# Kernel optimization log

Measured on AMD Instinct MI355X. Metric: run time of the kernel, lower is better.

The kernel has to match this reference:

```python
import jax, jax.numpy as jnp
import numpy as np

NH = 16   # neighbors
MD = 64   # model_dim
FF = 128  # ff_dim
H = 4     # heads
HD = MD // H
B, S, T = 2, 8192, 4096
LOG100 = float(np.log(100.0))


def _ln(x, g, b, eps=1e-5):
    m = x.mean(-1, keepdims=True)
    v = ((x - m) ** 2).mean(-1, keepdims=True)
    return (x - m) * jax.lax.rsqrt(v + eps) * g + b


def _lrelu(x):
    return jnp.where(x >= 0, x, 0.2 * x)


def setup_inputs():
    ks = jax.random.split(jax.random.key(0), 16)
    rn = lambda k, sh: jax.random.normal(k, sh, dtype=jnp.float32) * 0.05
    return {
        "x": jax.random.normal(ks[0], (B, S, 1), dtype=jnp.float32),
        "c1": jax.random.normal(ks[1], (B, S, T), dtype=jnp.float32),
        "c2": jax.random.normal(ks[2], (B, S, T), dtype=jnp.float32),
        "pe_W1": rn(ks[3], (2, FF)), "pe_b1": jnp.zeros((FF,), jnp.float32),
        "pe_W2": rn(ks[4], (FF, MD)), "pe_b2": jnp.zeros((MD,), jnp.float32),
        "Wq": rn(ks[5], (MD, MD)), "Wk": rn(ks[6], (MD, MD)), "Wv": rn(ks[7], (1, MD)),
        "logit_scale": jnp.full((H, 1, 1), float(np.log(10.0)), jnp.float32),
        "Wo": rn(ks[8], (MD, MD)), "bo": jnp.zeros((MD,), jnp.float32),
        "g1": jnp.ones((MD,), jnp.float32), "beta1": jnp.zeros((MD,), jnp.float32),
        "g2": jnp.ones((MD,), jnp.float32), "beta2": jnp.zeros((MD,), jnp.float32),
        "g3": jnp.ones((MD * NH,), jnp.float32), "beta3": jnp.zeros((MD * NH,), jnp.float32),
        "mnh_W1": rn(ks[9], (MD, FF)), "mnh_b1": jnp.zeros((FF,), jnp.float32),
        "mnh_W2": rn(ks[10], (FF, 1)), "mnh_b2": jnp.zeros((1,), jnp.float32),
        "mu_W1": rn(ks[11], (MD * NH, MD * NH)), "mu_b1": jnp.zeros((MD * NH,), jnp.float32),
        "mu_W2": rn(ks[12], (MD * NH, MD * NH)), "mu_b2": jnp.zeros((MD * NH,), jnp.float32),
    }


def reference(x, c1, c2, pe_W1, pe_b1, pe_W2, pe_b2, Wq, Wk, Wv, logit_scale, Wo, bo,
              g1, beta1, g2, beta2, g3, beta3,
              mnh_W1, mnh_b1, mnh_W2, mnh_b2, mu_W1, mu_b1, mu_W2, mu_b2):
    b, s, t = c1.shape
    # KNN over source axis s (cartesian distance), per target t
    d = c1 * c1 + c2 * c2                                  # [b,s,t]
    _, idx = jax.lax.top_k(-jnp.swapaxes(d, 1, 2), NH)     # [b,t,NH]
    x_nh = jax.vmap(lambda xb, ib: xb[ib])(x, idx)         # [b,t,NH,e]
    c1g = jnp.take_along_axis(jnp.swapaxes(c1, 1, 2), idx, axis=2)  # [b,t,NH]
    c2g = jnp.take_along_axis(jnp.swapaxes(c2, 1, 2), idx, axis=2)
    # relative-position embedding MLP (PE), already in [b,t,NH,MD] layout
    pe = jnp.stack([c1g, c2g], -1)                         # [b,t,NH,2]
    pe = jax.nn.gelu(pe @ pe_W1 + pe_b1) @ pe_W2 + pe_b2   # [b,t,NH,MD]
    h = _ln(x_nh + pe, g1, beta1).reshape(b * t, NH, MD)   # e=1 broadcasts
    v = jnp.einsum('bne,ed->bnd', x_nh.reshape(b * t, NH, 1), Wv)
    q = h @ Wq
    k = h @ Wk
    sp = lambda z: z.reshape(b * t, NH, H, HD).transpose(0, 2, 1, 3)
    qh, kh, vh = sp(q), sp(k), sp(v)
    # logit-scaled (cosine) attention over the NH neighbor axis
    qn = qh * jax.lax.rsqrt(jnp.sum(qh * qh, -1, keepdims=True) + 1e-12)
    kn = kh * jax.lax.rsqrt(jnp.sum(kh * kh, -1, keepdims=True) + 1e-12)
    scale = jnp.exp(jnp.minimum(logit_scale, LOG100))      # [H,1,1]
    att = jax.nn.softmax(jnp.einsum('bhnd,bhmd->bhnm', qn, kn) * scale, axis=-1)
    o = jnp.einsum('bhnm,bhmd->bhnd', att, vh).transpose(0, 2, 1, 3).reshape(b * t, NH, MD)
    h = _ln(h + (o @ Wo + bo), g2, beta2)
    # per-neighbor MLP producing a scalar, broadcast-added back
    h = h + _lrelu(_lrelu(h @ mnh_W1 + mnh_b1) @ mnh_W2 + mnh_b2)
    # unfold neighbors into channels and run the unfold MLP
    h = _ln(h.reshape(b, t, NH * MD), g3, beta3)
    return _lrelu(_lrelu(h @ mu_W1 + mu_b1) @ mu_W2 + mu_b2)  # [b,t,NH*MD]
```

## Files before the change

kernel.cpp:

```cpp
#include <hip/hip_runtime.h>
#include <hip/hip_bf16.h>

#define B_    2
#define SSRC  8192
#define TT    4096
#define NHN   16
#define NC    64
#define CS    128
#define LOG100D 4.605170185988091368035982909368

typedef short s16x8 __attribute__((ext_vector_type(8)));
typedef float f32x4 __attribute__((ext_vector_type(4)));
typedef double f64x4 __attribute__((ext_vector_type(4)));
typedef unsigned long long u64;

typedef const __attribute__((address_space(1))) void* gas_ptr;
typedef __attribute__((address_space(3))) void* las_ptr;
#define GLDS16(g, l) __builtin_amdgcn_global_load_lds((gas_ptr)(g), (las_ptr)(l), 16, 0, 0)

#define WFENCE asm volatile("s_waitcnt lgkmcnt(0)" ::: "memory")

__device__ __forceinline__ unsigned short f2bf(float f) {
    unsigned u = __float_as_uint(f);
    u = u + 0x7fffu + ((u >> 16) & 1u);
    return (unsigned short)(u >> 16);
}
__device__ __forceinline__ float bf2f(unsigned short h) {
    return __uint_as_float(((unsigned)h) << 16);
}
__device__ __forceinline__ double lrelu_d(double v) { return v >= 0.0 ? v : 0.2 * v; }
__device__ __forceinline__ double gelu_d(double u) {
    double a = 0.7978845608028654 * (u + 0.044715 * u * u * u);
    return 0.5 * u * (1.0 + tanh(a));
}
__device__ __forceinline__ double rsum16d(double v) {
    v += __shfl_xor(v, 1); v += __shfl_xor(v, 2);
    v += __shfl_xor(v, 4); v += __shfl_xor(v, 8);
    return v;
}
__device__ __forceinline__ double rmax16d(double v) {
    v = fmax(v, __shfl_xor(v, 1)); v = fmax(v, __shfl_xor(v, 2));
    v = fmax(v, __shfl_xor(v, 4)); v = fmax(v, __shfl_xor(v, 8));
    return v;
}
__device__ __forceinline__ double rsum64d(double v) {
    v += __shfl_xor(v, 1); v += __shfl_xor(v, 2); v += __shfl_xor(v, 4);
    v += __shfl_xor(v, 8); v += __shfl_xor(v, 16); v += __shfl_xor(v, 32);
    return v;
}

__device__ __forceinline__ int mfma64_discover() {
    int lane = threadIdx.x & 63;
    int l15 = lane & 15, lg = lane >> 4;
    double va = (double)(1 + ((lane * 37) % 61));
    double vb = (double)(2 + ((lane * 53) % 59));
    f64x4 d = (f64x4){0.0, 0.0, 0.0, 0.0};
    d = __builtin_amdgcn_mfma_f64_16x16x4f64(va, vb, d, 0, 0, 0);
    int found = -1;
#pragma unroll
    for (int c = 0; c < 8; c++) {
        int dm = (c >> 2) & 1, am = (c >> 1) & 1, bm = c & 1;
        bool ok = true;
#pragma unroll
        for (int r = 0; r < 4; r++) {
            int i = dm ? (lg + 4 * r) : (4 * lg + r);
            int j = l15;
            double e = 0.0;
#pragma unroll
            for (int k = 0; k < 4; k++) {
                int la = am ? (4 * i + k) : (i + 16 * k);
                int lb = bm ? (4 * j + k) : (j + 16 * k);
                e += (double)(1 + ((la * 37) % 61)) * (double)(2 + ((lb * 53) % 59));
            }
            ok = ok && (d[r] == e);
        }
        if (__all(ok) && found < 0) found = c;
    }
    return found;
}

__device__ __forceinline__ void ce(u64 &a, u64 &b) {
    bool c = a < b; u64 lo = c ? a : b; u64 hi = c ? b : a; a = lo; b = hi;
}
__device__ __forceinline__ void sort16(u64 (&k)[16]) {
    ce(k[0],k[8]); ce(k[1],k[9]); ce(k[2],k[10]); ce(k[3],k[11]);
    ce(k[4],k[12]); ce(k[5],k[13]); ce(k[6],k[14]); ce(k[7],k[15]);
    ce(k[0],k[4]); ce(k[1],k[5]); ce(k[2],k[6]); ce(k[3],k[7]);
    ce(k[8],k[12]); ce(k[9],k[13]); ce(k[10],k[14]); ce(k[11],k[15]);
    ce(k[4],k[8]); ce(k[5],k[9]); ce(k[6],k[10]); ce(k[7],k[11]);
    ce(k[0],k[2]); ce(k[1],k[3]); ce(k[4],k[6]); ce(k[5],k[7]);
    ce(k[8],k[10]); ce(k[9],k[11]); ce(k[12],k[14]); ce(k[13],k[15]);
    ce(k[2],k[8]); ce(k[3],k[9]); ce(k[6],k[12]); ce(k[7],k[13]);
    ce(k[2],k[4]); ce(k[3],k[5]); ce(k[6],k[8]); ce(k[7],k[9]);
    ce(k[10],k[12]); ce(k[11],k[13]);
    ce(k[0],k[1]); ce(k[2],k[3]); ce(k[4],k[5]); ce(k[6],k[7]);
    ce(k[8],k[9]); ce(k[10],k[11]); ce(k[12],k[13]); ce(k[14],k[15]);
    ce(k[1],k[8]); ce(k[3],k[10]); ce(k[5],k[12]); ce(k[7],k[14]);
    ce(k[1],k[4]); ce(k[3],k[6]); ce(k[5],k[8]); ce(k[7],k[10]);
    ce(k[9],k[12]); ce(k[11],k[14]);
    ce(k[1],k[2]); ce(k[3],k[4]); ce(k[5],k[6]); ce(k[7],k[8]);
    ce(k[9],k[10]); ce(k[11],k[12]); ce(k[13],k[14]);
}
__device__ __forceinline__ void bmerge16(u64 (&k)[16]) {
    ce(k[0],k[8]); ce(k[1],k[9]); ce(k[2],k[10]); ce(k[3],k[11]);
    ce(k[4],k[12]); ce(k[5],k[13]); ce(k[6],k[14]); ce(k[7],k[15]);
    ce(k[0],k[4]); ce(k[1],k[5]); ce(k[2],k[6]); ce(k[3],k[7]);
    ce(k[8],k[12]); ce(k[9],k[13]); ce(k[10],k[14]); ce(k[11],k[15]);
    ce(k[0],k[2]); ce(k[1],k[3]); ce(k[4],k[6]); ce(k[5],k[7]);
    ce(k[8],k[10]); ce(k[9],k[11]); ce(k[12],k[14]); ce(k[13],k[15]);
    ce(k[0],k[1]); ce(k[2],k[3]); ce(k[4],k[5]); ce(k[6],k[7]);
    ce(k[8],k[9]); ce(k[10],k[11]); ce(k[12],k[13]); ce(k[14],k[15]);
}
__device__ __forceinline__ void merge_keep16(u64 (&L)[16], const u64 (&B)[16]) {
#pragma unroll
    for (int i = 0; i < 16; i++) { u64 bb = B[15 - i]; L[i] = L[i] < bb ? L[i] : bb; }
    bmerge16(L);
}

__global__ __launch_bounds__(256) void topk_partial(
    const float* __restrict__ c1, const float* __restrict__ c2,
    u64* __restrict__ cand)
{
    int t = blockIdx.x * 256 + threadIdx.x;
    int ch = blockIdx.y, b = blockIdx.z;
    const float* p1 = c1 + ((size_t)b * SSRC + (size_t)ch * CS) * TT + t;
    const float* p2 = c2 + ((size_t)b * SSRC + (size_t)ch * CS) * TT + t;
    u64 k[16];
#pragma unroll
    for (int j = 0; j < 16; j++) k[j] = ~0ull;
    int sbase = ch * CS;
    for (int s = 0; s < CS; s += 16) {
        u64 bt[16];
#pragma unroll
        for (int u = 0; u < 16; u++) {
            float a_ = p1[(size_t)(s + u) * TT];
            float b_ = p2[(size_t)(s + u) * TT];
            float dd = __fadd_rn(__fmul_rn(a_, a_), __fmul_rn(b_, b_));
            bt[u] = ((u64)__float_as_uint(dd) << 32) | (unsigned)(sbase + s + u);
        }
        sort16(bt);
        merge_keep16(k, bt);
    }
    u64* dst = cand + ((size_t)(b * NC + ch) * 16) * TT + t;
#pragma unroll
    for (int j = 0; j < 16; j++) dst[(size_t)j * TT] = k[j];
}

__global__ __launch_bounds__(64) void topk_merge1(
    const u64* __restrict__ cand, u64* __restrict__ c2c)
{
    int t = blockIdx.x * 64 + threadIdx.x;
    int g = blockIdx.y, b = blockIdx.z;
    u64 k[16];
#pragma unroll
    for (int j = 0; j < 16; j++) k[j] = ~0ull;
    for (int c = g * 8; c < g * 8 + 8; c++) {
        const u64* src = cand + ((size_t)(b * NC + c) * 16) * TT + t;
        u64 bt[16];
#pragma unroll
        for (int j = 0; j < 16; j++) bt[j] = src[(size_t)j * TT];
        merge_keep16(k, bt);
    }
    u64* dst = c2c + ((size_t)((b * 8 + g) * 16)) * TT + t;
#pragma unroll
    for (int j = 0; j < 16; j++) dst[(size_t)j * TT] = k[j];
}

__global__ __launch_bounds__(64) void topk_merge2(
    const u64* __restrict__ c2c, int* __restrict__ knn)
{
    int t = blockIdx.x * 64 + threadIdx.x;
    int b = blockIdx.y;
    u64 k[16];
#pragma unroll
    for (int j = 0; j < 16; j++) k[j] = ~0ull;
    for (int c = 0; c < 8; c++) {
        const u64* src = c2c + ((size_t)(b * 8 + c) * 16) * TT + t;
        u64 bt[16];
#pragma unroll
        for (int j = 0; j < 16; j++) bt[j] = src[(size_t)j * TT];
        merge_keep16(k, bt);
    }
#pragma unroll
    for (int j = 0; j < 16; j++)
        knn[((size_t)b * TT + t) * 16 + j] = (int)(unsigned)(k[j] & 0xffffffffull);
}

__global__ __launch_bounds__(256) void wconv(
    const float* __restrict__ Wa, const float* __restrict__ Wb,
    unsigned short* __restrict__ Oah, unsigned short* __restrict__ Oal,
    unsigned short* __restrict__ Obh, unsigned short* __restrict__ Obl)
{
    const float* W = blockIdx.z ? Wb : Wa;
    unsigned short* Oh = blockIdx.z ? Obh : Oah;
    unsigned short* Ol = blockIdx.z ? Obl : Oal;
    __shared__ float tile[64][65];
    int tx = threadIdx.x & 63, ty = threadIdx.x >> 6;
    int n0 = blockIdx.x * 64, k0 = blockIdx.y * 64;
#pragma unroll
    for (int r = ty; r < 64; r += 4) tile[r][tx] = W[(size_t)(k0 + r) * 1024 + n0 + tx];
    __syncthreads();
#pragma unroll
    for (int r = ty; r < 64; r += 4) {
        float v = tile[tx][r];
        unsigned short hi = f2bf(v);
        Oh[(size_t)(n0 + r) * 1024 + k0 + tx] = hi;
        Ol[(size_t)(n0 + r) * 1024 + k0 + tx] = f2bf(v - bf2f(hi));
    }
}

__global__ __launch_bounds__(256) void tok_pe_m(
    const float* __restrict__ x, const float* __restrict__ c1, const float* __restrict__ c2,
    const int* __restrict__ knn,
    const float* __restrict__ peW1, const float* __restrict__ peb1,
    const float* __restrict__ peW2, const float* __restrict__ peb2,
    const float* __restrict__ g1, const float* __restrict__ be1,
    float* __restrict__ hout)
{
    int cand = mfma64_discover();
    if (cand < 0) return;
    __shared__ float s_peW1[256], s_peb1[128], s_peW2[8448], s_peb2[64], s_g1[64], s_be1[64];
    __shared__ float s_scr[4][2352];
    int tid = threadIdx.x, lane = tid & 63, w = tid >> 6;
    if (tid < 256) s_peW1[tid] = peW1[tid];
    if (tid < 128) s_peb1[tid] = peb1[tid];
    if (tid < 64) { s_peb2[tid] = peb2[tid]; s_g1[tid] = g1[tid]; s_be1[tid] = be1[tid]; }
    for (int i = tid; i < 8192; i += 256) s_peW2[(i >> 6) * 66 + (i & 63)] = peW2[i];
    __syncthreads();

    int l15 = lane & 15, lg = lane >> 4;
    int am = (cand >> 1) & 1, bm = cand & 1, dm = (cand >> 2) & 1;
    int a_i = am ? (lane >> 2) : l15;
    int a_k = am ? (lane & 3)  : lg;
    int b_k = bm ? (lane & 3)  : lg;
    int b_j = bm ? (lane >> 2) : l15;
    int i0 = dm ? lg : 4 * lg;
    int istep = dm ? 4 : 1;

    float* big = s_scr[w];
    float* sc1 = big + 2304; float* sc2 = big + 2320; float* sx = big + 2336;
    double w0a = s_peW1[lane], w1a = s_peW1[128 + lane], ba = s_peb1[lane];
    double w0b = s_peW1[64 + lane], w1b = s_peW1[192 + lane], bbv = s_peb1[64 + lane];
    double g1v[4], be1v[4], pb2v[4];
#pragma unroll
    for (int j = 0; j < 4; j++) {
        g1v[j]  = (double)s_g1[j * 16 + l15];
        be1v[j] = (double)s_be1[j * 16 + l15];
        pb2v[j] = (double)s_peb2[j * 16 + l15];
    }

    for (int it = 0; it < 4; ++it) {
        int tk = blockIdx.x * 16 + w * 4 + it;
        int bb = tk >> 12, tt = tk & (TT - 1);
        if (lane < 16) {
            int s = knn[(size_t)tk * 16 + lane];
            sc1[lane] = c1[((size_t)bb * SSRC + s) * TT + tt];
            sc2[lane] = c2[((size_t)bb * SSRC + s) * TT + tt];
            sx[lane]  = x[bb * SSRC + s];
        }
        WFENCE;
#pragma unroll
        for (int n = 0; n < 16; n++) {
            double a_ = (double)sc1[n], b_ = (double)sc2[n];
            big[lane * 18 + n]        = (float)gelu_d(a_ * w0a + b_ * w1a + ba);
            big[(lane + 64) * 18 + n] = (float)gelu_d(a_ * w0b + b_ * w1b + bbv);
        }
        WFENCE;
        f64x4 acc[4];
#pragma unroll
        for (int j = 0; j < 4; j++) acc[j] = (f64x4){0.0, 0.0, 0.0, 0.0};
        for (int ks = 0; ks < 32; ks++) {
            double a = (double)big[(4 * ks + a_k) * 18 + a_i];
            const float* wrow = &s_peW2[(4 * ks + b_k) * 66 + b_j];
#pragma unroll
            for (int j = 0; j < 4; j++)
                acc[j] = __builtin_amdgcn_mfma_f64_16x16x4f64(a, (double)wrow[j * 16], acc[j], 0, 0, 0);
        }
        float* op = hout + (size_t)tk * 1024;
#pragma unroll
        for (int r = 0; r < 4; r++) {
            int n = i0 + istep * r;
            double xr = (double)sx[n];
            double v[4], s = 0.0;
#pragma unroll
            for (int j = 0; j < 4; j++) { v[j] = acc[j][r] + pb2v[j] + xr; s += v[j]; }
            double m = rsum16d(s) * (1.0 / 64.0);
            double q = 0.0;
#pragma unroll
            for (int j = 0; j < 4; j++) { double d = v[j] - m; q += d * d; }
            double var = rsum16d(q) * (1.0 / 64.0);
            double rs = sqrt(var + 1e-5);
#pragma unroll
            for (int j = 0; j < 4; j++)
                op[n * 64 + j * 16 + l15] = (float)((v[j] - m) / rs * g1v[j] + be1v[j]);
        }
    }
}

__global__ __launch_bounds__(256) void tok_pe_v(
    const float* __restrict__ x, const float* __restrict__ c1, const float* __restrict__ c2,
    const int* __restrict__ knn,
    const float* __restrict__ peW1, const float* __restrict__ peb1,
    const float* __restrict__ peW2, const float* __restrict__ peb2,
    const float* __restrict__ g1, const float* __restrict__ be1,
    float* __restrict__ hout)
{
    int cand = mfma64_discover();
    if (cand >= 0) return;
    __shared__ float s_peW1[256], s_peb1[128], s_peW2[8448], s_peb2[64], s_g1[64], s_be1[64];
    __shared__ float s_scr[4][2352];
    int tid = threadIdx.x, lane = tid & 63, w = tid >> 6;
    if (tid < 256) s_peW1[tid] = peW1[tid];
    if (tid < 128) s_peb1[tid] = peb1[tid];
    if (tid < 64) { s_peb2[tid] = peb2[tid]; s_g1[tid] = g1[tid]; s_be1[tid] = be1[tid]; }
    for (int i = tid; i < 8192; i += 256) s_peW2[(i >> 6) * 66 + (i & 63)] = peW2[i];
    __syncthreads();

    float* big = s_scr[w];
    float* sc1 = big + 2304; float* sc2 = big + 2320; float* sx = big + 2336;
    double w0a = s_peW1[lane], w1a = s_peW1[128 + lane], ba = s_peb1[lane];
    double w0b = s_peW1[64 + lane], w1b = s_peW1[192 + lane], bbv = s_peb1[64 + lane];
    double gv = (double)s_g1[lane], bv = (double)s_be1[lane];
    double pb2 = (double)s_peb2[lane];

    for (int it = 0; it < 4; ++it) {
        int tk = blockIdx.x * 16 + w * 4 + it;
        int bb = tk >> 12, tt = tk & (TT - 1);
        if (lane < 16) {
            int s = knn[(size_t)tk * 16 + lane];
            sc1[lane] = c1[((size_t)bb * SSRC + s) * TT + tt];
            sc2[lane] = c2[((size_t)bb * SSRC + s) * TT + tt];
            sx[lane]  = x[bb * SSRC + s];
        }
        WFENCE;
#pragma unroll
        for (int n = 0; n < 16; n++) {
            double a_ = (double)sc1[n], b_ = (double)sc2[n];
            big[lane * 18 + n]        = (float)gelu_d(a_ * w0a + b_ * w1a + ba);
            big[(lane + 64) * 18 + n] = (float)gelu_d(a_ * w0b + b_ * w1b + bbv);
        }
        WFENCE;
        double acc[16];
#pragma unroll
        for (int n = 0; n < 16; n++) acc[n] = pb2;
        for (int f = 0; f < 128; f++) {
            double wv = (double)s_peW2[f * 66 + lane];
#pragma unroll
            for (int n = 0; n < 16; n += 2) {
                float2 gvv = *(const float2*)&big[f * 18 + n];
                acc[n]     += (double)gvv.x * wv;
                acc[n + 1] += (double)gvv.y * wv;
            }
        }
        float* op = hout + (size_t)tk * 1024 + lane;
#pragma unroll
        for (int n = 0; n < 16; n++) {
            double v = acc[n] + (double)sx[n];
            double m = rsum64d(v) * (1.0 / 64.0);
            double d = v - m;
            double var = rsum64d(d * d) * (1.0 / 64.0);
            op[n * 64] = (float)(d / sqrt(var + 1e-5) * gv + bv);
        }
    }
}

__global__ __launch_bounds__(256) void tok_attn(
    const float* __restrict__ x, const int* __restrict__ knn,
    const float* __restrict__ Wq, const float* __restrict__ Wk,
    const float* __restrict__ Wv, const float* __restrict__ lsc,
    const float* __restrict__ Wo, const float* __restrict__ bo,
    const float* __restrict__ g2, const float* __restrict__ be2,
    float* __restrict__ hio)
{
    __shared__ float s_Wq[4224], s_Wk[4224], s_WoV[256], s_bo[64], s_g2[64], s_be2[64];
    __shared__ float s_scr[4][2320];
    int tid = threadIdx.x, lane = tid & 63, w = tid >> 6;
    if (tid < 64) {
        s_bo[tid] = bo[tid]; s_g2[tid] = g2[tid]; s_be2[tid] = be2[tid];
        for (int hh = 0; hh < 4; hh++) {
            double a = 0.0;
            for (int hd = 0; hd < 16; hd++)
                a += (double)Wv[hh * 16 + hd] * (double)Wo[(hh * 16 + hd) * 64 + tid];
            s_WoV[hh * 64 + tid] = (float)a;
        }
    }
    for (int i = tid; i < 4096; i += 256) {
        s_Wq[(i >> 6) * 66 + (i & 63)] = Wq[i];
        s_Wk[(i >> 6) * 66 + (i & 63)] = Wk[i];
    }
    __syncthreads();

    int head = lane >> 4, mm = lane & 15;
    double scaleh = exp(fmin((double)lsc[head], LOG100D));
    double wov0 = (double)s_WoV[lane], wov1 = (double)s_WoV[64 + lane];
    double wov2 = (double)s_WoV[128 + lane], wov3 = (double)s_WoV[192 + lane];
    double gv = (double)s_g2[lane], bv = (double)s_be2[lane], bov = (double)s_bo[lane];
    float* big = s_scr[w];
    float* sx = big + 2304;

    for (int it = 0; it < 4; ++it) {
        int tk = blockIdx.x * 16 + w * 4 + it;
        int bb = tk >> 12;
        if (lane < 16) {
            int s = knn[(size_t)tk * 16 + lane];
            sx[lane] = x[bb * SSRC + s];
        }
        float* hp = hio + (size_t)tk * 1024 + lane;
        double h[16];
#pragma unroll
        for (int n = 0; n < 16; n++) {
            h[n] = (double)hp[n * 64];
            big[lane * 18 + n] = (float)h[n];
        }
        WFENCE;
        double q[16], k2[16];
#pragma unroll
        for (int n = 0; n < 16; n++) { q[n] = 0.0; k2[n] = 0.0; }
        for (int kk = 0; kk < 64; kk++) {
            double wq = (double)s_Wq[kk * 66 + lane], wk = (double)s_Wk[kk * 66 + lane];
#pragma unroll
            for (int n = 0; n < 16; n += 2) {
                float2 hv = *(const float2*)&big[kk * 18 + n];
                q[n]  += (double)hv.x * wq; q[n + 1]  += (double)hv.y * wq;
                k2[n] += (double)hv.x * wk; k2[n + 1] += (double)hv.y * wk;
            }
        }
#pragma unroll
        for (int n = 0; n < 16; n++) {
            double sq = rsum16d(q[n] * q[n]);   q[n]  /= sqrt(sq + 1e-12);
            double sk = rsum16d(k2[n] * k2[n]); k2[n] /= sqrt(sk + 1e-12);
        }
        WFENCE;
#pragma unroll
        for (int n = 0; n < 16; n++) {
            big[lane * 18 + n]        = (float)q[n];
            big[1152 + lane * 18 + n] = (float)k2[n];
        }
        WFENCE;
        double A_[16];
        {
            double S[16];
#pragma unroll
            for (int n = 0; n < 16; n++) S[n] = 0.0;
            for (int hd = 0; hd < 16; hd++) {
                int r = head * 16 + hd;
                double kf = (double)big[1152 + r * 18 + mm];
#pragma unroll
                for (int n = 0; n < 16; n += 2) {
                    float2 qq = *(const float2*)&big[r * 18 + n];
                    S[n] += (double)qq.x * kf; S[n + 1] += (double)qq.y * kf;
                }
            }
            double xv = (double)sx[mm];
#pragma unroll
            for (int n = 0; n < 16; n++) {
                double sv = S[n] * scaleh;
                double mx = rmax16d(sv);
                double e = exp(sv - mx);
                double se = rsum16d(e);
                A_[n] = rsum16d((e / se) * xv);
            }
        }
#pragma unroll
        for (int n = 0; n < 16; n++) {
            double a0 = __shfl(A_[n], mm), a1 = __shfl(A_[n], 16 + mm);
            double a2 = __shfl(A_[n], 32 + mm), a3 = __shfl(A_[n], 48 + mm);
            double v = h[n] + a0 * wov0 + a1 * wov1 + a2 * wov2 + a3 * wov3 + bov;
            double m = rsum64d(v) * (1.0 / 64.0);
            double d = v - m;
            double var = rsum64d(d * d) * (1.0 / 64.0);
            hp[n * 64] = (float)(d / sqrt(var + 1e-5) * gv + bv);
        }
    }
}

__global__ __launch_bounds__(256) void tok_mnh_m(
    const float* __restrict__ hin,
    const float* __restrict__ mW1, const float* __restrict__ mb1,
    const float* __restrict__ mW2, const float* __restrict__ mb2,
    const float* __restrict__ g3, const float* __restrict__ be3,
    unsigned short* __restrict__ hnh, unsigned short* __restrict__ hnl)
{
    int cand = mfma64_discover();
    if (cand < 0) return;
    __shared__ float s_mW1[8320], s_mb1[128], s_mW2[128], s_g3[1024], s_be3[1024];
    __shared__ float s_scr[4][1152];
    int tid = threadIdx.x, lane = tid & 63, w = tid >> 6;
    if (tid < 128) { s_mb1[tid] = mb1[tid]; s_mW2[tid] = mW2[tid]; }
    for (int i = tid; i < 8192; i += 256) s_mW1[(i >> 7) * 130 + (i & 127)] = mW1[i];
    for (int i = tid; i < 1024; i += 256) { s_g3[i] = g3[i]; s_be3[i] = be3[i]; }
    __syncthreads();

    int l15 = lane & 15, lg = lane >> 4;
    int am = (cand >> 1) & 1, bm = cand & 1, dm = (cand >> 2) & 1;
    int a_i = am ? (lane >> 2) : l15;
    int a_k = am ? (lane & 3)  : lg;
    int b_k = bm ? (lane & 3)  : lg;
    int b_j = bm ? (lane >> 2) : l15;

    double mb2s = (double)mb2[0];
    double mb1v[8], w2v[8];
#pragma unroll
    for (int j = 0; j < 8; j++) {
        mb1v[j] = (double)s_mb1[j * 16 + l15];
        w2v[j]  = (double)s_mW2[j * 16 + l15];
    }
    float* big = s_scr[w];

    for (int it = 0; it < 4; ++it) {
        int tk = blockIdx.x * 16 + w * 4 + it;
        const float* hp = hin + (size_t)tk * 1024 + lane;
        double h[16];
#pragma unroll
        for (int n = 0; n < 16; n++) {
            h[n] = (double)hp[n * 64];
            big[lane * 18 + n] = (float)h[n];
        }
        WFENCE;
        f64x4 acc[8];
#pragma unroll
        for (int j = 0; j < 8; j++) acc[j] = (f64x4){0.0, 0.0, 0.0, 0.0};
        for (int ks = 0; ks < 16; ks++) {
            double a = (double)big[(4 * ks + a_k) * 18 + a_i];
            const float* wrow = &s_mW1[(4 * ks + b_k) * 130 + b_j];
#pragma unroll
            for (int j = 0; j < 8; j++)
                acc[j] = __builtin_amdgcn_mfma_f64_16x16x4f64(a, (double)wrow[j * 16], acc[j], 0, 0, 0);
        }
        double p[4];
#pragma unroll
        for (int r = 0; r < 4; r++) {
            double s = 0.0;
#pragma unroll
            for (int j = 0; j < 8; j++) {
                double t = acc[j][r] + mb1v[j];
                s += lrelu_d(t) * w2v[j];
            }
            p[r] = rsum16d(s);
        }
        if (dm == 0) {
#pragma unroll
            for (int n = 0; n < 16; n++) {
                double pn = __shfl(p[n & 3], (n >> 2) * 16);
                h[n] += lrelu_d(pn + mb2s);
            }
        } else {
#pragma unroll
            for (int n = 0; n < 16; n++) {
                double pn = __shfl(p[n >> 2], (n & 3) * 16);
                h[n] += lrelu_d(pn + mb2s);
            }
        }
        double s1 = 0.0;
#pragma unroll
        for (int n = 0; n < 16; n++) s1 += h[n];
        s1 = rsum64d(s1) * (1.0 / 1024.0);
        double s2v = 0.0;
#pragma unroll
        for (int n = 0; n < 16; n++) { double d = h[n] - s1; s2v += d * d; }
        s2v = rsum64d(s2v) * (1.0 / 1024.0);
        double rs = 1.0 / sqrt(s2v + 1e-5);
        unsigned short* oph = hnh + (size_t)tk * 1024 + lane;
        unsigned short* opl = hnl + (size_t)tk * 1024 + lane;
#pragma unroll
        for (int n = 0; n < 16; n++) {
            double v = (h[n] - s1) * rs * (double)s_g3[n * 64 + lane] + (double)s_be3[n * 64 + lane];
            unsigned short hi = f2bf((float)v);
            oph[n * 64] = hi;
            opl[n * 64] = f2bf((float)(v - (double)bf2f(hi)));
        }
    }
}

__global__ __launch_bounds__(256) void tok_mnh_v(
    const float* __restrict__ hin,
    const float* __restrict__ mW1, const float* __restrict__ mb1,
    const float* __restrict__ mW2, const float* __restrict__ mb2,
    const float* __restrict__ g3, const float* __restrict__ be3,
    unsigned short* __restrict__ hnh, unsigned short* __restrict__ hnl)
{
    int cand = mfma64_discover();
    if (cand >= 0) return;
    __shared__ float s_mW1[8320], s_mb1[128], s_mW2[128], s_g3[1024], s_be3[1024];
    __shared__ float s_scr[4][1152];
    int tid = threadIdx.x, lane = tid & 63, w = tid >> 6;
    if (tid < 128) { s_mb1[tid] = mb1[tid]; s_mW2[tid] = mW2[tid]; }
    for (int i = tid; i < 8192; i += 256) s_mW1[(i >> 7) * 130 + (i & 127)] = mW1[i];
    for (int i = tid; i < 1024; i += 256) { s_g3[i] = g3[i]; s_be3[i] = be3[i]; }
    __syncthreads();

    double mb2s = (double)mb2[0];
    double mb1a = (double)s_mb1[lane], mb1b = (double)s_mb1[64 + lane];
    double w2a = (double)s_mW2[lane], w2b = (double)s_mW2[64 + lane];
    float* big = s_scr[w];

    for (int it = 0; it < 4; ++it) {
        int tk = blockIdx.x * 16 + w * 4 + it;
        const float* hp = hin + (size_t)tk * 1024 + lane;
        double h[16];
#pragma unroll
        for (int n = 0; n < 16; n++) {
            h[n] = (double)hp[n * 64];
            big[lane * 18 + n] = (float)h[n];
        }
        WFENCE;
        double t1a[16], t1b[16];
#pragma unroll
        for (int n = 0; n < 16; n++) { t1a[n] = mb1a; t1b[n] = mb1b; }
        for (int kk = 0; kk < 64; kk++) {
            double wa = (double)s_mW1[kk * 130 + lane], wb = (double)s_mW1[kk * 130 + 64 + lane];
#pragma unroll
            for (int n = 0; n < 16; n += 2) {
                float2 hv = *(const float2*)&big[kk * 18 + n];
                t1a[n] += (double)hv.x * wa; t1a[n + 1] += (double)hv.y * wa;
                t1b[n] += (double)hv.x * wb; t1b[n + 1] += (double)hv.y * wb;
            }
        }
#pragma unroll
        for (int n = 0; n < 16; n++) {
            double p = lrelu_d(t1a[n]) * w2a + lrelu_d(t1b[n]) * w2b;
            p = rsum64d(p);
            h[n] += lrelu_d(p + mb2s);
        }
        double s1 = 0.0;
#pragma unroll
        for (int n = 0; n < 16; n++) s1 += h[n];
        s1 = rsum64d(s1) * (1.0 / 1024.0);
        double s2v = 0.0;
#pragma unroll
        for (int n = 0; n < 16; n++) { double d = h[n] - s1; s2v += d * d; }
        s2v = rsum64d(s2v) * (1.0 / 1024.0);
        double rs = 1.0 / sqrt(s2v + 1e-5);
        unsigned short* oph = hnh + (size_t)tk * 1024 + lane;
        unsigned short* opl = hnl + (size_t)tk * 1024 + lane;
#pragma unroll
        for (int n = 0; n < 16; n++) {
            double v = (h[n] - s1) * rs * (double)s_g3[n * 64 + lane] + (double)s_be3[n * 64 + lane];
            unsigned short hi = f2bf((float)v);
            oph[n * 64] = hi;
            opl[n * 64] = f2bf((float)(v - (double)bf2f(hi)));
        }
    }
}

#define AH_OFF 0
#define AL_OFF 4096
#define BH_OFF 8192
#define BL_OFF 12288
template<int OUTSPLIT>
__global__ __launch_bounds__(256) void gemm_split(
    const unsigned short* __restrict__ Ah, const unsigned short* __restrict__ Al,
    const unsigned short* __restrict__ Bh, const unsigned short* __restrict__ Bl,
    const float* __restrict__ bias,
    unsigned short* __restrict__ oh, unsigned short* __restrict__ ol,
    float* __restrict__ of, int M, int N, int K)
{
    __shared__ unsigned short SM[16384];
    int tid = threadIdx.x, lane = tid & 63, w = tid >> 6;
    int wm = w >> 1, wn = w & 1;
    int m0 = blockIdx.y * 128, n0 = blockIdx.x * 128;
    f32x4 acc[4][4];
#pragma unroll
    for (int i = 0; i < 4; i++)
#pragma unroll
        for (int j = 0; j < 4; j++) acc[i][j] = (f32x4){0.f, 0.f, 0.f, 0.f};
    int row = tid >> 2, c8 = (tid & 3) * 8;
    size_t aoff = (size_t)(m0 + row) * K + c8;
    size_t boff = (size_t)(n0 + row) * K + c8;
    for (int kk = 0; kk < K; kk += 32) {
        __syncthreads();
        GLDS16(Ah + aoff + kk,                   SM + AH_OFF + tid * 8);
        GLDS16(Ah + aoff + (size_t)64 * K + kk,  SM + AH_OFF + 2048 + tid * 8);
        GLDS16(Al + aoff + kk,                   SM + AL_OFF + tid * 8);
        GLDS16(Al + aoff + (size_t)64 * K + kk,  SM + AL_OFF + 2048 + tid * 8);
        GLDS16(Bh + boff + kk,                   SM + BH_OFF + tid * 8);
        GLDS16(Bh + boff + (size_t)64 * K + kk,  SM + BH_OFF + 2048 + tid * 8);
        GLDS16(Bl + boff + kk,                   SM + BL_OFF + tid * 8);
        GLDS16(Bl + boff + (size_t)64 * K + kk,  SM + BL_OFF + 2048 + tid * 8);
        asm volatile("s_waitcnt vmcnt(0)" ::: "memory");
        __syncthreads();
        int kh = (lane >> 4) * 8, rA = wm * 64 + (lane & 15), rB = wn * 64 + (lane & 15);
        s16x8 afh[4], afl[4], bfh[4], bfl[4];
#pragma unroll
        for (int i = 0; i < 4; i++) {
            afh[i] = *(const s16x8*)&SM[AH_OFF + (rA + i * 16) * 32 + kh];
            afl[i] = *(const s16x8*)&SM[AL_OFF + (rA + i * 16) * 32 + kh];
            bfh[i] = *(const s16x8*)&SM[BH_OFF + (rB + i * 16) * 32 + kh];
            bfl[i] = *(const s16x8*)&SM[BL_OFF + (rB + i * 16) * 32 + kh];
        }
#pragma unroll
        for (int i = 0; i < 4; i++)
#pragma unroll
            for (int j = 0; j < 4; j++) {
                acc[i][j] = __builtin_amdgcn_mfma_f32_16x16x32_bf16(afl[i], bfh[j], acc[i][j], 0, 0, 0);
                acc[i][j] = __builtin_amdgcn_mfma_f32_16x16x32_bf16(afh[i], bfl[j], acc[i][j], 0, 0, 0);
                acc[i][j] = __builtin_amdgcn_mfma_f32_16x16x32_bf16(afh[i], bfh[j], acc[i][j], 0, 0, 0);
            }
    }
    float bc[4];
#pragma unroll
    for (int j = 0; j < 4; j++) bc[j] = bias[n0 + wn * 64 + j * 16 + (lane & 15)];
#pragma unroll
    for (int i = 0; i < 4; i++) {
#pragma unroll
        for (int j = 0; j < 4; j++) {
#pragma unroll
            for (int r = 0; r < 4; r++) {
                int rw = m0 + wm * 64 + i * 16 + (lane >> 4) * 4 + r;
                int cl = n0 + wn * 64 + j * 16 + (lane & 15);
                float v = acc[i][j][r] + bc[j];
                v = v >= 0.f ? v : 0.2f * v;
                if (OUTSPLIT) {
                    unsigned short hi = f2bf(v);
                    oh[(size_t)rw * N + cl] = hi;
                    ol[(size_t)rw * N + cl] = f2bf(v - bf2f(hi));
                } else {
                    of[(size_t)rw * N + cl] = v;
                }
            }
        }
    }
}

extern "C" void kernel_launch(void* const* d_in, const int* in_sizes, int n_in,
                              void* d_out, int out_size, void* d_ws, size_t ws_size,
                              hipStream_t stream)
{
    const float* x    = (const float*)d_in[0];
    const float* c1   = (const float*)d_in[1];
    const float* c2   = (const float*)d_in[2];
    const float* peW1 = (const float*)d_in[3];
    const float* peb1 = (const float*)d_in[4];
    const float* peW2 = (const float*)d_in[5];
    const float* peb2 = (const float*)d_in[6];
    const float* Wq   = (const float*)d_in[7];
    const float* Wk   = (const float*)d_in[8];
    const float* Wv   = (const float*)d_in[9];
    const float* lsc  = (const float*)d_in[10];
    const float* Wo   = (const float*)d_in[11];
    const float* bo   = (const float*)d_in[12];
    const float* g1   = (const float*)d_in[13];
    const float* be1  = (const float*)d_in[14];
    const float* g2   = (const float*)d_in[15];
    const float* be2  = (const float*)d_in[16];
    const float* g3   = (const float*)d_in[17];
    const float* be3  = (const float*)d_in[18];
    const float* mW1  = (const float*)d_in[19];
    const float* mb1  = (const float*)d_in[20];
    const float* mW2  = (const float*)d_in[21];
    const float* mb2  = (const float*)d_in[22];
    const float* muW1 = (const float*)d_in[23];
    const float* mub1 = (const float*)d_in[24];
    const float* muW2 = (const float*)d_in[25];
    const float* mub2 = (const float*)d_in[26];

    const size_t MB = (size_t)1 << 20;
    char* ws = (char*)d_ws;
    u64*            cand   = (u64*)(ws);
    float*          hbuf   = (float*)(ws);
    unsigned short* y1h    = (unsigned short*)(ws);
    unsigned short* y1l    = (unsigned short*)(ws + 16 * MB);
    unsigned short* hnh    = (unsigned short*)(ws + 32 * MB);
    unsigned short* hnl    = (unsigned short*)(ws + 48 * MB);
    u64*            c2c    = (u64*)(ws + 64 * MB);
    unsigned short* w1th   = (unsigned short*)(ws + 72 * MB);
    unsigned short* w1tl   = (unsigned short*)(ws + 74 * MB);
    unsigned short* w2th   = (unsigned short*)(ws + 76 * MB);
    unsigned short* w2tl   = (unsigned short*)(ws + 78 * MB);
    int*            knn    = (int*)(ws + 80 * MB);
    (void)in_sizes; (void)n_in; (void)out_size; (void)ws_size;

    wconv<<<dim3(16, 16, 2), 256, 0, stream>>>(muW1, muW2, w1th, w1tl, w2th, w2tl);
    topk_partial<<<dim3(TT / 256, NC, B_), 256, 0, stream>>>(c1, c2, cand);
    topk_merge1<<<dim3(TT / 64, 8, B_), 64, 0, stream>>>(cand, c2c);
    topk_merge2<<<dim3(TT / 64, B_), 64, 0, stream>>>(c2c, knn);
    tok_pe_m<<<dim3(512), 256, 0, stream>>>(x, c1, c2, knn, peW1, peb1, peW2, peb2, g1, be1, hbuf);
    tok_pe_v<<<dim3(512), 256, 0, stream>>>(x, c1, c2, knn, peW1, peb1, peW2, peb2, g1, be1, hbuf);
    tok_attn<<<dim3(512), 256, 0, stream>>>(x, knn, Wq, Wk, Wv, lsc, Wo, bo, g2, be2, hbuf);
    tok_mnh_m<<<dim3(512), 256, 0, stream>>>(hbuf, mW1, mb1, mW2, mb2, g3, be3, hnh, hnl);
    tok_mnh_v<<<dim3(512), 256, 0, stream>>>(hbuf, mW1, mb1, mW2, mb2, g3, be3, hnh, hnl);
    gemm_split<1><<<dim3(8, 64), 256, 0, stream>>>(hnh, hnl, w1th, w1tl, mub1,
                                                   y1h, y1l, (float*)nullptr, 8192, 1024, 1024);
    gemm_split<0><<<dim3(8, 64), 256, 0, stream>>>(y1h, y1l, w2th, w2tl, mub2,
                                                   (unsigned short*)nullptr, (unsigned short*)nullptr,
                                                   (float*)d_out, 8192, 1024, 1024);
}
```

Baseline: 706.7 us.

## Split attention Q/K projection into separate FP64 MFMA kernel with scratch buffers

Moves the Q and K projections plus their normalisation out of the fused attention kernel into a new kernel. That kernel uses FP64 16x16x4 MFMA when runtime discovery finds a usable layout and keeps a scalar FP64 fallback otherwise. The normalised q and k are written to global scratch, and the remaining attention kernel reads them back. Work runs in two halves of tokens so the scratch fits in the workspace. This aims to replace the scalar double FMA loop with matrix instructions, at the cost of extra global traffic and more kernel launches.

```diff
diff --git a/kernel.cpp b/kernel.cpp
--- a/kernel.cpp
+++ b/kernel.cpp
@@ -364,15 +364,130 @@
     }
 }
 
-__global__ __launch_bounds__(256) void tok_attn(
+__global__ __launch_bounds__(256) void tok_attn1_m(
+    const float* __restrict__ hin,
+    const float* __restrict__ Wq, const float* __restrict__ Wk,
+    float* __restrict__ qng, float* __restrict__ kng, int t0)
+{
+    int cand = mfma64_discover();
+    if (cand < 0) return;
+    __shared__ float s_Wq[4224], s_Wk[4224];
+    __shared__ float s_scr[4][1152];
+    int tid = threadIdx.x, lane = tid & 63, w = tid >> 6;
+    for (int i = tid; i < 4096; i += 256) {
+        s_Wq[(i >> 6) * 66 + (i & 63)] = Wq[i];
+        s_Wk[(i >> 6) * 66 + (i & 63)] = Wk[i];
+    }
+    __syncthreads();
+
+    int l15 = lane & 15, lg = lane >> 4;
+    int am = (cand >> 1) & 1, bm = cand & 1, dm = (cand >> 2) & 1;
+    int a_i = am ? (lane >> 2) : l15;
+    int a_k = am ? (lane & 3)  : lg;
+    int b_k = bm ? (lane & 3)  : lg;
+    int b_j = bm ? (lane >> 2) : l15;
+    int i0 = dm ? lg : 4 * lg;
+    int istep = dm ? 4 : 1;
+    float* big = s_scr[w];
+
+    for (int it = 0; it < 4; ++it) {
+        int tk = t0 + blockIdx.x * 16 + w * 4 + it;
+        int tl = tk - t0;
+        const float* hp = hin + (size_t)tk * 1024 + lane;
+#pragma unroll
+        for (int n = 0; n < 16; n++) big[lane * 18 + n] = hp[n * 64];
+        WFENCE;
+        f64x4 qa[4], ka[4];
+#pragma unroll
+        for (int j = 0; j < 4; j++) { qa[j] = (f64x4){0.,0.,0.,0.}; ka[j] = (f64x4){0.,0.,0.,0.}; }
+        for (int ks = 0; ks < 16; ks++) {
+            double a = (double)big[(4 * ks + a_k) * 18 + a_i];
+            const float* wq = &s_Wq[(4 * ks + b_k) * 66 + b_j];
+            const float* wk = &s_Wk[(4 * ks + b_k) * 66 + b_j];
+#pragma unroll
+            for (int j = 0; j < 4; j++) {
+                qa[j] = __builtin_amdgcn_mfma_f64_16x16x4f64(a, (double)wq[j * 16], qa[j], 0, 0, 0);
+                ka[j] = __builtin_amdgcn_mfma_f64_16x16x4f64(a, (double)wk[j * 16], ka[j], 0, 0, 0);
+            }
+        }
+        WFENCE;
+        float* qp = qng + (size_t)tl * 1024;
+        float* kp = kng + (size_t)tl * 1024;
+#pragma unroll
+        for (int j = 0; j < 4; j++) {
+#pragma unroll
+            for (int r = 0; r < 4; r++) {
+                double qq = qa[j][r], kk2 = ka[j][r];
+                double sq = rsum16d(qq * qq);
+                double sk = rsum16d(kk2 * kk2);
+                qq  /= sqrt(sq + 1e-12);
+                kk2 /= sqrt(sk + 1e-12);
+                int n = i0 + istep * r;
+                qp[n * 64 + j * 16 + l15] = (float)qq;
+                kp[n * 64 + j * 16 + l15] = (float)kk2;
+            }
+        }
+    }
+}
+
+__global__ __launch_bounds__(256) void tok_attn1_v(
+    const float* __restrict__ hin,
+    const float* __restrict__ Wq, const float* __restrict__ Wk,
+    float* __restrict__ qng, float* __restrict__ kng, int t0)
+{
+    int cand = mfma64_discover();
+    if (cand >= 0) return;
+    __shared__ float s_Wq[4224], s_Wk[4224];
+    __shared__ float s_scr[4][1152];
+    int tid = threadIdx.x, lane = tid & 63, w = tid >> 6;
+    for (int i = tid; i < 4096; i += 256) {
+        s_Wq[(i >> 6) * 66 + (i & 63)] = Wq[i];
+        s_Wk[(i >> 6) * 66 + (i & 63)] = Wk[i];
+    }
+    __syncthreads();
+    float* big = s_scr[w];
+
+    for (int it = 0; it < 4; ++it) {
+        int tk = t0 + blockIdx.x * 16 + w * 4 + it;
+        int tl = tk - t0;
+        const float* hp = hin + (size_t)tk * 1024 + lane;
+#pragma unroll
+        for (int n = 0; n < 16; n++) big[lane * 18 + n] = hp[n * 64];
+        WFENCE;
+        double q[16], k2[16];
+#pragma unroll
+        for (int n = 0; n < 16; n++) { q[n] = 0.0; k2[n] = 0.0; }
+        for (int kk = 0; kk < 64; kk++) {
+            double wq = (double)s_Wq[kk * 66 + lane], wk = (double)s_Wk[kk * 66 + lane];
+#pragma unroll
+            for (int n = 0; n < 16; n += 2) {
+                float2 hv = *(const float2*)&big[kk * 18 + n];
+                q[n]  += (double)hv.x * wq; q[n + 1]  += (double)hv.y * wq;
+                k2[n] += (double)hv.x * wk; k2[n + 1] += (double)hv.y * wk;
+            }
+        }
+        WFENCE;
+        float* qp = qng + (size_t)tl * 1024 + lane;
+        float* kp = kng + (size_t)tl * 1024 + lane;
+#pragma unroll
+        for (int n = 0; n < 16; n++) {
+            double sq = rsum16d(q[n] * q[n]);   q[n]  /= sqrt(sq + 1e-12);
+            double sk = rsum16d(k2[n] * k2[n]); k2[n] /= sqrt(sk + 1e-12);
+            qp[n * 64] = (float)q[n];
+            kp[n * 64] = (float)k2[n];
+        }
+    }
+}
+
+__global__ __launch_bounds__(256) void tok_attn2(
     const float* __restrict__ x, const int* __restrict__ knn,
-    const float* __restrict__ Wq, const float* __restrict__ Wk,
+    const float* __restrict__ qng, const float* __restrict__ kng,
     const float* __restrict__ Wv, const float* __restrict__ lsc,
     const float* __restrict__ Wo, const float* __restrict__ bo,
     const float* __restrict__ g2, const float* __restrict__ be2,
-    float* __restrict__ hio)
-{
-    __shared__ float s_Wq[4224], s_Wk[4224], s_WoV[256], s_bo[64], s_g2[64], s_be2[64];
+    float* __restrict__ hio, int t0)
+{
+    __shared__ float s_WoV[256], s_bo[64], s_g2[64], s_be2[64];
     __shared__ float s_scr[4][2320];
     int tid = threadIdx.x, lane = tid & 63, w = tid >> 6;
     if (tid < 64) {
@@ -384,10 +499,6 @@
             s_WoV[hh * 64 + tid] = (float)a;
         }
     }
-    for (int i = tid; i < 4096; i += 256) {
-        s_Wq[(i >> 6) * 66 + (i & 63)] = Wq[i];
-        s_Wk[(i >> 6) * 66 + (i & 63)] = Wk[i];
-    }
     __syncthreads();
 
     int head = lane >> 4, mm = lane & 15;
@@ -399,7 +510,8 @@
     float* sx = big + 2304;
 
     for (int it = 0; it < 4; ++it) {
-        int tk = blockIdx.x * 16 + w * 4 + it;
+        int tk = t0 + blockIdx.x * 16 + w * 4 + it;
+        int tl = tk - t0;
         int bb = tk >> 12;
         if (lane < 16) {
             int s = knn[(size_t)tk * 16 + lane];
@@ -408,33 +520,13 @@
         float* hp = hio + (size_t)tk * 1024 + lane;
         double h[16];
 #pragma unroll
-        for (int n = 0; n < 16; n++) {
-            h[n] = (double)hp[n * 64];
-            big[lane * 18 + n] = (float)h[n];
-        }
-        WFENCE;
-        double q[16], k2[16];
-#pragma unroll
-        for (int n = 0; n < 16; n++) { q[n] = 0.0; k2[n] = 0.0; }
-        for (int kk = 0; kk < 64; kk++) {
-            double wq = (double)s_Wq[kk * 66 + lane], wk = (double)s_Wk[kk * 66 + lane];
-#pragma unroll
-            for (int n = 0; n < 16; n += 2) {
-                float2 hv = *(const float2*)&big[kk * 18 + n];
-                q[n]  += (double)hv.x * wq; q[n + 1]  += (double)hv.y * wq;
-                k2[n] += (double)hv.x * wk; k2[n + 1] += (double)hv.y * wk;
-            }
-        }
-#pragma unroll
-        for (int n = 0; n < 16; n++) {
-            double sq = rsum16d(q[n] * q[n]);   q[n]  /= sqrt(sq + 1e-12);
-            double sk = rsum16d(k2[n] * k2[n]); k2[n] /= sqrt(sk + 1e-12);
-        }
-        WFENCE;
-#pragma unroll
-        for (int n = 0; n < 16; n++) {
-            big[lane * 18 + n]        = (float)q[n];
-            big[1152 + lane * 18 + n] = (float)k2[n];
+        for (int n = 0; n < 16; n++) h[n] = (double)hp[n * 64];
+        const float* qp = qng + (size_t)tl * 1024 + lane;
+        const float* kp = kng + (size_t)tl * 1024 + lane;
+#pragma unroll
+        for (int n = 0; n < 16; n++) {
+            big[lane * 18 + n]        = qp[n * 64];
+            big[1152 + lane * 18 + n] = kp[n * 64];
         }
         WFENCE;
         double A_[16];
@@ -760,6 +852,8 @@
     float*          hbuf   = (float*)(ws);
     unsigned short* y1h    = (unsigned short*)(ws);
     unsigned short* y1l    = (unsigned short*)(ws + 16 * MB);
+    float*          qng    = (float*)(ws + 32 * MB);
+    float*          kng    = (float*)(ws + 48 * MB);
     unsigned short* hnh    = (unsigned short*)(ws + 32 * MB);
     unsigned short* hnl    = (unsigned short*)(ws + 48 * MB);
     u64*            c2c    = (u64*)(ws + 64 * MB);
@@ -776,7 +870,12 @@
     topk_merge2<<<dim3(TT / 64, B_), 64, 0, stream>>>(c2c, knn);
     tok_pe_m<<<dim3(512), 256, 0, stream>>>(x, c1, c2, knn, peW1, peb1, peW2, peb2, g1, be1, hbuf);
     tok_pe_v<<<dim3(512), 256, 0, stream>>>(x, c1, c2, knn, peW1, peb1, peW2, peb2, g1, be1, hbuf);
-    tok_attn<<<dim3(512), 256, 0, stream>>>(x, knn, Wq, Wk, Wv, lsc, Wo, bo, g2, be2, hbuf);
+    for (int t0 = 0; t0 < 8192; t0 += 4096) {
+        tok_attn1_m<<<dim3(256), 256, 0, stream>>>(hbuf, Wq, Wk, qng, kng, t0);
+        tok_attn1_v<<<dim3(256), 256, 0, stream>>>(hbuf, Wq, Wk, qng, kng, t0);
+        tok_attn2<<<dim3(256), 256, 0, stream>>>(x, knn, qng, kng, Wv, lsc, Wo, bo,
+                                                 g2, be2, hbuf, t0);
+    }
     tok_mnh_m<<<dim3(512), 256, 0, stream>>>(hbuf, mW1, mb1, mW2, mb2, g3, be3, hnh, hnl);
     tok_mnh_v<<<dim3(512), 256, 0, stream>>>(hbuf, mW1, mb1, mW2, mb2, g3, be3, hnh, hnl);
     gemm_split<1><<<dim3(8, 64), 256, 0, stream>>>(hnh, hnl, w1th, w1tl, mub1,
```

New measurement: 780.5 us. 1.1x slower.
